# Kernel tuning notes

Measured on AMD Instinct MI355X. Metric: run time of the kernel, lower is better.

Reference implementation:

```python
import jax, jax.numpy as jnp
import numpy as np

B, Fc, C, H, D, L = 128, 256, 256, 8, 32, 6  # batch, columns, dim, heads, head_dim, layers


def _ln(x, g, b, eps=1e-5):
    m = x.mean(-1, keepdims=True)
    v = ((x - m) ** 2).mean(-1, keepdims=True)
    return (x - m) * jax.lax.rsqrt(v + eps) * g + b


def setup_inputs() -> dict:
    key = jax.random.key(0)
    ks = jax.random.split(key, 16)
    s = 0.02  # weight init scale to keep 6-layer activations stable
    return {
        "x": jax.random.normal(ks[0], (B, Fc, C), jnp.float32),
        "col_emb": jax.random.normal(ks[1], (1, Fc, C), jnp.float32),
        "pos_emb": jax.random.normal(ks[2], (1, Fc + 1, C), jnp.float32),
        "col_bias": jax.random.normal(ks[3], (Fc, Fc), jnp.float32),
        "ln1_g": jnp.ones((L, C), jnp.float32),
        "ln1_b": jnp.zeros((L, C), jnp.float32),
        "qkv_w": jax.random.normal(ks[4], (L, C, 3 * C), jnp.float32) * s,
        "qkv_b": jnp.zeros((L, 3 * C), jnp.float32),
        "out_w": jax.random.normal(ks[5], (L, C, C), jnp.float32) * s,
        "out_b": jnp.zeros((L, C), jnp.float32),
        "ln2_g": jnp.ones((L, C), jnp.float32),
        "ln2_b": jnp.zeros((L, C), jnp.float32),
        "w1": jax.random.normal(ks[6], (L, C, 4 * C), jnp.float32) * s,
        "b1": jnp.zeros((L, 4 * C), jnp.float32),
        "w2": jax.random.normal(ks[7], (L, 4 * C, 2 * C), jnp.float32) * s,
        "b2": jnp.zeros((L, 2 * C), jnp.float32),
        "w3": jax.random.normal(ks[8], (L, C, C), jnp.float32) * s,
        "b3": jnp.zeros((L, C), jnp.float32),
        "fin_g": jnp.ones((C,), jnp.float32),
        "fin_b": jnp.zeros((C,), jnp.float32),
    }


def reference(x, col_emb, pos_emb, col_bias, ln1_g, ln1_b, qkv_w, qkv_b,
              out_w, out_b, ln2_g, ln2_b, w1, b1, w2, b2, w3, b3, fin_g, fin_b):
    Fdim = x.shape[1]
    h = x + col_emb[:, :Fdim] + pos_emb[:, 1:Fdim + 1]
    bias = col_bias[:Fdim, :Fdim]  # [T, T]
    scale = 1.0 / np.sqrt(D).astype(np.float32)
    params = (ln1_g, ln1_b, qkv_w, qkv_b, out_w, out_b, ln2_g, ln2_b,
              w1, b1, w2, b2, w3, b3)

    def block(xc, p):
        g1, be1, qw, qb, ow, ob, g2, be2, W1, B1, W2, B2, W3, B3 = p
        Bn, T, Cd = xc.shape
        hn = _ln(xc, g1, be1)
        qkv = hn @ qw + qb                              # [B,T,3C]
        q, k, v = jnp.split(qkv, 3, axis=-1)
        q = q.reshape(Bn, T, H, D)
        k = k.reshape(Bn, T, H, D)
        v = v.reshape(Bn, T, H, D)
        scores = jnp.einsum('bthd,bshd->bhts', q, k) * scale + bias[None, None]
        w = jax.nn.softmax(scores, axis=-1)             # dropout = identity (eval)
        attn = jnp.einsum('bhts,bshd->bthd', w, v).reshape(Bn, T, Cd)
        attn = attn @ ow + ob
        attn = attn + bias[None]                        # [1,T,T] broadcast, T==C
        xc = xc + attn
        hn2 = _ln(xc, g2, be2)
        u = jax.nn.gelu(hn2 @ W1 + B1, approximate=False)
        gl = u @ W2 + B2                                # [B,T,2C]
        a, gate = jnp.split(gl, 2, axis=-1)
        xc = xc + (a * jax.nn.sigmoid(gate)) @ W3 + B3
        return xc, None

    h, _ = jax.lax.scan(block, h, params)
    h = _ln(h, fin_g, fin_b)
    return h.mean(axis=1)  # pooling='mean' -> [B, C]
```

## Files before the change

kernel.cpp:

```cpp
#include <hip/hip_runtime.h>

typedef __bf16 bx8 __attribute__((ext_vector_type(8)));
typedef float fx4 __attribute__((ext_vector_type(4)));

#define GAS(p) ((const __attribute__((address_space(1))) void*)(const void*)(p))
#define LAS(p) ((__attribute__((address_space(3))) void*)(void*)(p))
#define WAITVM(n) do { asm volatile("s_waitcnt vmcnt(" #n ")" ::: "memory"); \
                       __builtin_amdgcn_sched_barrier(0); } while (0)
#define WAITLG0() do { asm volatile("s_waitcnt lgkmcnt(0)" ::: "memory"); \
                       __builtin_amdgcn_sched_barrier(0); } while (0)

__device__ __forceinline__ unsigned short f2bf(float f) {
  return __builtin_bit_cast(unsigned short, (__bf16)f);
}

__global__ __launch_bounds__(256) void wtrans_kernel(const float* __restrict__ src,
                                                     unsigned short* __restrict__ dst,
                                                     int K, int N) {
  __shared__ unsigned short t[64][68];
  const int l = blockIdx.z;
  const float* s = src + (size_t)l * K * N;
  unsigned short* d = dst + (size_t)l * N * K;
  const int n0 = blockIdx.x * 64, k0 = blockIdx.y * 64;
  const int tx = threadIdx.x & 63, ty = threadIdx.x >> 6;
#pragma unroll
  for (int r = 0; r < 64; r += 4)
    t[tx][ty + r] = f2bf(s[(size_t)(k0 + ty + r) * N + n0 + tx]);
  __syncthreads();
#pragma unroll
  for (int r = 0; r < 64; r += 4)
    d[(size_t)(n0 + ty + r) * K + k0 + tx] = t[ty + r][tx];
}

__global__ __launch_bounds__(256) void embed_ln_kernel(const float4* __restrict__ x,
                                                       const float4* __restrict__ ce,
                                                       const float4* __restrict__ pe,
                                                       const float* __restrict__ gw,
                                                       const float* __restrict__ bw,
                                                       float4* __restrict__ xres,
                                                       unsigned short* __restrict__ hn) {
  const int row = blockIdx.x * 4 + (threadIdx.x >> 6);
  const int lane = threadIdx.x & 63;
  const int t = row & 255;
  const size_t idx = (size_t)row * 64 + lane;
  float4 a = x[idx], b = ce[t * 64 + lane], p = pe[(t + 1) * 64 + lane];
  float4 v = make_float4(a.x + b.x + p.x, a.y + b.y + p.y, a.z + b.z + p.z, a.w + b.w + p.w);
  xres[idx] = v;
  float s = v.x + v.y + v.z + v.w;
  float q = v.x * v.x + v.y * v.y + v.z * v.z + v.w * v.w;
#pragma unroll
  for (int off = 1; off < 64; off <<= 1) {
    s += __shfl_xor(s, off);
    q += __shfl_xor(q, off);
  }
  float mean = s * (1.0f / 256.0f);
  float rs = rsqrtf(q * (1.0f / 256.0f) - mean * mean + 1e-5f);
  float4 gv = *(const float4*)(gw + lane * 4);
  float4 bv = *(const float4*)(bw + lane * 4);
  ushort4 o;
  o.x = f2bf((v.x - mean) * rs * gv.x + bv.x);
  o.y = f2bf((v.y - mean) * rs * gv.y + bv.y);
  o.z = f2bf((v.z - mean) * rs * gv.z + bv.z);
  o.w = f2bf((v.w - mean) * rs * gv.w + bv.w);
  *(ushort4*)(hn + (size_t)row * 256 + lane * 4) = o;
}

__global__ __launch_bounds__(256) void mean_part_kernel(const float* __restrict__ x,
                                                        const float2* __restrict__ stats,
                                                        float* __restrict__ part) {
  int b = blockIdx.x, half = blockIdx.y, c = threadIdx.x;
  const float* xb = x + (size_t)b * 65536 + half * 32768;
  const float2* st = stats + b * 256 + half * 128;
  float acc = 0.f;
#pragma unroll 4
  for (int t = 0; t < 128; ++t) {
    float2 s = st[t];
    acc += (xb[t * 256 + c] - s.x) * s.y;
  }
  part[(size_t)(b * 2 + half) * 256 + c] = acc;
}
__global__ __launch_bounds__(256) void mean_fin_kernel(const float* __restrict__ part,
                                                       const float* __restrict__ fg,
                                                       const float* __restrict__ fb,
                                                       float* __restrict__ out) {
  int b = blockIdx.x, c = threadIdx.x;
  out[b * 256 + c] =
      (part[(size_t)(2 * b) * 256 + c] + part[(size_t)(2 * b + 1) * 256 + c]) *
          (1.0f / 256.0f) * fg[c] + fb[c];
}

template <int EP>
__global__ __launch_bounds__(256) void gemm_kernel(const unsigned short* __restrict__ A,
                                                   const unsigned short* __restrict__ BT,
                                                   const float* __restrict__ bvec,
                                                   float* __restrict__ resid,
                                                   unsigned short* __restrict__ outb,
                                                   int N, int K) {
  __shared__ unsigned short lA[2][128 * 32];
  __shared__ unsigned short lB[2][128 * 32];
  const int tid = threadIdx.x;
  const int lane = tid & 63, w = tid >> 6;
  const int wr = w >> 1, wc = w & 1;
  const int g = lane >> 4, lr = lane & 15;
  const int m0 = blockIdx.y * 128, n0 = blockIdx.x * 128;
  fx4 acc[4][4] = {};

  auto STAGE = [&](int buf, int kk) {
#pragma unroll
    for (int r = 0; r < 2; ++r) {
      int u = r * 256 + tid;
      int row = u >> 2, sl = u & 3;
      int c = sl ^ ((row >> 1) & 3);
      __builtin_amdgcn_global_load_lds(GAS(A + (size_t)(m0 + row) * K + kk + c * 8),
                                       LAS(&lA[buf][u * 8]), 16, 0, 0);
      __builtin_amdgcn_global_load_lds(GAS(BT + (size_t)(n0 + row) * K + kk + c * 8),
                                       LAS(&lB[buf][u * 8]), 16, 0, 0);
    }
  };

  const int nt = K >> 5;
  STAGE(0, 0);
  STAGE(1, 32);
  for (int t = 0; t < nt; ++t) {
    if (t == nt - 1) WAITVM(0); else WAITVM(4);
    __builtin_amdgcn_s_barrier();
    const int buf = t & 1;
    bx8 af[4], bq[4];
#pragma unroll
    for (int i = 0; i < 4; ++i) {
      int row = wr * 64 + i * 16 + lr;
      af[i] = *(const bx8*)&lA[buf][row * 32 + (g ^ ((row >> 1) & 3)) * 8];
      int col = wc * 64 + i * 16 + lr;
      bq[i] = *(const bx8*)&lB[buf][col * 32 + (g ^ ((col >> 1) & 3)) * 8];
    }
    WAITLG0();
    __builtin_amdgcn_s_barrier();
    if (t + 2 < nt) STAGE(buf, (t + 2) * 32);
#pragma unroll
    for (int i = 0; i < 4; ++i)
#pragma unroll
      for (int j = 0; j < 4; ++j)
        acc[i][j] = __builtin_amdgcn_mfma_f32_16x16x32_bf16(bq[j], af[i], acc[i][j], 0, 0, 0);
  }

#pragma unroll
  for (int i = 0; i < 4; ++i) {
    const int m = m0 + wr * 64 + i * 16 + lr;
#pragma unroll
    for (int j = 0; j < 4; ++j) {
      const int nc = n0 + wc * 64 + j * 16 + g * 4;
      const float4 bv = *(const float4*)(bvec + nc);
      float v0 = acc[i][j][0] + bv.x, v1 = acc[i][j][1] + bv.y;
      float v2 = acc[i][j][2] + bv.z, v3 = acc[i][j][3] + bv.w;
      if constexpr (EP == 1) {
        v0 = 0.5f * v0 * (1.0f + erff(v0 * 0.70710678118654752f));
        v1 = 0.5f * v1 * (1.0f + erff(v1 * 0.70710678118654752f));
        v2 = 0.5f * v2 * (1.0f + erff(v2 * 0.70710678118654752f));
        v3 = 0.5f * v3 * (1.0f + erff(v3 * 0.70710678118654752f));
      }
      if constexpr (EP == 1) {
        ushort4 st;
        st.x = f2bf(v0); st.y = f2bf(v1); st.z = f2bf(v2); st.w = f2bf(v3);
        *(ushort4*)(outb + (size_t)m * N + nc) = st;
      } else {
        if (nc < 512) {
          ushort4 st;
          st.x = f2bf(v0); st.y = f2bf(v1); st.z = f2bf(v2); st.w = f2bf(v3);
          *(ushort4*)(outb + (size_t)m * N + nc) = st;
        } else {
          unsigned short* vTp = (unsigned short*)resid;
          const int s = m & 255, b = m >> 8;
          const int hv = nc - 512;
          const int h = hv >> 5, d0 = hv & 31;
          const int jj = (s & 3) + 4 * ((s >> 4) & 1);
          const int ub = (s >> 5) * 128 + ((s >> 2) & 3) * 32 + d0;
          unsigned short* base = vTp + (size_t)(b * 8 + h) * 8192;
          const float vv[4] = {v0, v1, v2, v3};
#pragma unroll
          for (int r = 0; r < 4; ++r) {
            int u = ub + r;
            int up = (u & ~7) | ((u & 7) ^ ((u >> 3) & 7));
            base[up * 8 + jj] = f2bf(vv[r]);
          }
        }
      }
    }
  }
}

template <int EP, int LNM>
__global__ __launch_bounds__(256) void gemm_ln_kernel(const unsigned short* __restrict__ A,
                                                      const unsigned short* __restrict__ BT,
                                                      const float* __restrict__ bvec,
                                                      const float* __restrict__ cbias,
                                                      float* __restrict__ resid,
                                                      const float* __restrict__ lnw,
                                                      const float* __restrict__ lnb,
                                                      unsigned short* __restrict__ hn,
                                                      float2* __restrict__ stats,
                                                      int K) {
  __shared__ unsigned short lA[2][32 * 32];
  __shared__ unsigned short lB[2][256 * 32];
  __shared__ float2 red[4][32];
  const int tid = threadIdx.x;
  const int lane = tid & 63, w = tid >> 6;
  const int g = lane >> 4, lr = lane & 15;
  const int m0 = blockIdx.x * 32;
  fx4 acc[2][4] = {};

  auto STAGE = [&](int buf, int kk) {
    {
      int u = tid & 127;
      int row = u >> 2, sl = u & 3;
      int c = sl ^ ((row >> 1) & 3);
      __builtin_amdgcn_global_load_lds(GAS(A + (size_t)(m0 + row) * K + kk + c * 8),
                                       LAS(&lA[buf][u * 8]), 16, 0, 0);
    }
#pragma unroll
    for (int r = 0; r < 4; ++r) {
      int u = r * 256 + tid;
      int row = u >> 2, sl = u & 3;
      int c = sl ^ ((row >> 1) & 3);
      __builtin_amdgcn_global_load_lds(GAS(BT + (size_t)row * K + kk + c * 8),
                                       LAS(&lB[buf][u * 8]), 16, 0, 0);
    }
  };

  const int nt = K >> 5;
  STAGE(0, 0);
  STAGE(1, 32);
  for (int t = 0; t < nt; ++t) {
    if (t == nt - 1) WAITVM(0); else WAITVM(5);
    __builtin_amdgcn_s_barrier();
    const int buf = t & 1;
    bx8 af[2], bq[4];
#pragma unroll
    for (int i = 0; i < 2; ++i) {
      int row = i * 16 + lr;
      af[i] = *(const bx8*)&lA[buf][row * 32 + (g ^ ((row >> 1) & 3)) * 8];
    }
#pragma unroll
    for (int j = 0; j < 4; ++j) {
      int col = w * 64 + j * 16 + lr;
      bq[j] = *(const bx8*)&lB[buf][col * 32 + (g ^ ((col >> 1) & 3)) * 8];
    }
    WAITLG0();
    __builtin_amdgcn_s_barrier();
    if (t + 2 < nt) STAGE(buf, (t + 2) * 32);
#pragma unroll
    for (int i = 0; i < 2; ++i)
#pragma unroll
      for (int j = 0; j < 4; ++j)
        acc[i][j] = __builtin_amdgcn_mfma_f32_16x16x32_bf16(bq[j], af[i], acc[i][j], 0, 0, 0);
  }

  float s[2] = {0.f, 0.f}, q[2] = {0.f, 0.f};
#pragma unroll
  for (int i = 0; i < 2; ++i) {
    const int m = m0 + i * 16 + lr;
#pragma unroll
    for (int j = 0; j < 4; ++j) {
      const int nc = w * 64 + j * 16 + g * 4;
      const float4 bv = *(const float4*)(bvec + nc);
      float v0 = acc[i][j][0] + bv.x, v1 = acc[i][j][1] + bv.y;
      float v2 = acc[i][j][2] + bv.z, v3 = acc[i][j][3] + bv.w;
      if constexpr (EP == 2) {
        const float4 cb = *(const float4*)(cbias + (size_t)(m & 255) * 256 + nc);
        v0 += cb.x; v1 += cb.y; v2 += cb.z; v3 += cb.w;
      }
      float4* rp = (float4*)(resid + (size_t)m * 256 + nc);
      float4 old = *rp;
      v0 += old.x; v1 += old.y; v2 += old.z; v3 += old.w;
      *rp = make_float4(v0, v1, v2, v3);
      acc[i][j][0] = v0; acc[i][j][1] = v1; acc[i][j][2] = v2; acc[i][j][3] = v3;
      s[i] += v0 + v1 + v2 + v3;
      q[i] += v0 * v0 + v1 * v1 + v2 * v2 + v3 * v3;
    }
  }
#pragma unroll
  for (int i = 0; i < 2; ++i) {
    s[i] += __shfl_xor(s[i], 16); s[i] += __shfl_xor(s[i], 32);
    q[i] += __shfl_xor(q[i], 16); q[i] += __shfl_xor(q[i], 32);
  }
  if (lane < 16) {
#pragma unroll
    for (int i = 0; i < 2; ++i) red[w][i * 16 + lr] = make_float2(s[i], q[i]);
  }
  __syncthreads();
  float mean[2], rs[2];
#pragma unroll
  for (int i = 0; i < 2; ++i) {
    float2 r0 = red[0][i * 16 + lr], r1 = red[1][i * 16 + lr];
    float2 r2 = red[2][i * 16 + lr], r3 = red[3][i * 16 + lr];
    float S = r0.x + r1.x + r2.x + r3.x;
    float Q = r0.y + r1.y + r2.y + r3.y;
    mean[i] = S * (1.0f / 256.0f);
    rs[i] = rsqrtf(Q * (1.0f / 256.0f) - mean[i] * mean[i] + 1e-5f);
  }
  if constexpr (LNM == 1) {
    if (w == 0 && g == 0) {
#pragma unroll
      for (int i = 0; i < 2; ++i) stats[m0 + i * 16 + lr] = make_float2(mean[i], rs[i]);
    }
  } else {
#pragma unroll
    for (int i = 0; i < 2; ++i) {
      const int m = m0 + i * 16 + lr;
#pragma unroll
      for (int j = 0; j < 4; ++j) {
        const int nc = w * 64 + j * 16 + g * 4;
        const float4 gv = *(const float4*)(lnw + nc);
        const float4 bv2 = *(const float4*)(lnb + nc);
        ushort4 st;
        st.x = f2bf((acc[i][j][0] - mean[i]) * rs[i] * gv.x + bv2.x);
        st.y = f2bf((acc[i][j][1] - mean[i]) * rs[i] * gv.y + bv2.y);
        st.z = f2bf((acc[i][j][2] - mean[i]) * rs[i] * gv.z + bv2.z);
        st.w = f2bf((acc[i][j][3] - mean[i]) * rs[i] * gv.w + bv2.w);
        *(ushort4*)(hn + (size_t)m * 256 + nc) = st;
      }
    }
  }
}

__global__ __launch_bounds__(256) void gemm_w2f64_kernel(const unsigned short* __restrict__ A,
                                                         const unsigned short* __restrict__ BT,
                                                         const float* __restrict__ b2,
                                                         unsigned short* __restrict__ gout) {
  __shared__ unsigned short lA[3][64 * 32];
  __shared__ unsigned short lBa[3][128 * 32];
  __shared__ unsigned short lBg[3][128 * 32];
  const int tid = threadIdx.x;
  const int lane = tid & 63, w = tid >> 6;
  const int g = lane >> 4, lr = lane & 15;
  const int m0 = blockIdx.y * 64, n0 = blockIdx.x * 128;
  fx4 aA[4][2] = {}, aG[4][2] = {};

  auto STAGE = [&](int buf, int kk) {
    {
      int u = tid;
      int row = u >> 2, sl = u & 3;
      int c = sl ^ ((row >> 1) & 3);
      __builtin_amdgcn_global_load_lds(GAS(A + (size_t)(m0 + row) * 1024 + kk + c * 8),
                                       LAS(&lA[buf][u * 8]), 16, 0, 0);
    }
#pragma unroll
    for (int r = 0; r < 2; ++r) {
      int u = r * 256 + tid;
      int row = u >> 2, sl = u & 3;
      int c = sl ^ ((row >> 1) & 3);
      __builtin_amdgcn_global_load_lds(GAS(BT + (size_t)(n0 + row) * 1024 + kk + c * 8),
                                       LAS(&lBa[buf][u * 8]), 16, 0, 0);
      __builtin_amdgcn_global_load_lds(GAS(BT + (size_t)(256 + n0 + row) * 1024 + kk + c * 8),
                                       LAS(&lBg[buf][u * 8]), 16, 0, 0);
    }
  };

  STAGE(0, 0);
  STAGE(1, 32);
  STAGE(2, 64);
  int buf = 0;
  for (int t = 0; t < 32; ++t) {
    if (t < 30) WAITVM(10); else if (t == 30) WAITVM(5); else WAITVM(0);
    __builtin_amdgcn_s_barrier();
    bx8 af[4], ba[2], bg[2];
#pragma unroll
    for (int i = 0; i < 4; ++i) {
      int row = i * 16 + lr;
      af[i] = *(const bx8*)&lA[buf][row * 32 + (g ^ ((row >> 1) & 3)) * 8];
    }
#pragma unroll
    for (int j = 0; j < 2; ++j) {
      int col = w * 32 + j * 16 + lr;
      int sw = (g ^ ((col >> 1) & 3)) * 8;
      ba[j] = *(const bx8*)&lBa[buf][col * 32 + sw];
      bg[j] = *(const bx8*)&lBg[buf][col * 32 + sw];
    }
    WAITLG0();
    __builtin_amdgcn_s_barrier();
    if (t + 3 < 32) STAGE(buf, (t + 3) * 32);
#pragma unroll
    for (int i = 0; i < 4; ++i)
#pragma unroll
      for (int j = 0; j < 2; ++j) {
        aA[i][j] = __builtin_amdgcn_mfma_f32_16x16x32_bf16(ba[j], af[i], aA[i][j], 0, 0, 0);
        aG[i][j] = __builtin_amdgcn_mfma_f32_16x16x32_bf16(bg[j], af[i], aG[i][j], 0, 0, 0);
      }
    buf = (buf == 2) ? 0 : buf + 1;
  }

#pragma unroll
  for (int i = 0; i < 4; ++i) {
    const int m = m0 + i * 16 + lr;
#pragma unroll
    for (int j = 0; j < 2; ++j) {
      const int nc = n0 + w * 32 + j * 16 + g * 4;
      const float4 bva = *(const float4*)(b2 + nc);
      const float4 bvg = *(const float4*)(b2 + 256 + nc);
      float a0 = aA[i][j][0] + bva.x, a1 = aA[i][j][1] + bva.y;
      float a2 = aA[i][j][2] + bva.z, a3 = aA[i][j][3] + bva.w;
      float g0 = aG[i][j][0] + bvg.x, g1 = aG[i][j][1] + bvg.y;
      float g2 = aG[i][j][2] + bvg.z, g3 = aG[i][j][3] + bvg.w;
      ushort4 st;
      st.x = f2bf(a0 / (1.0f + __expf(-g0)));
      st.y = f2bf(a1 / (1.0f + __expf(-g1)));
      st.z = f2bf(a2 / (1.0f + __expf(-g2)));
      st.w = f2bf(a3 / (1.0f + __expf(-g3)));
      *(ushort4*)(gout + (size_t)m * 256 + nc) = st;
    }
  }
}

__global__ __launch_bounds__(256) void attn_kernel(const unsigned short* __restrict__ qkv,
                                                   const unsigned short* __restrict__ vT,
                                                   const float* __restrict__ cbias,
                                                   unsigned short* __restrict__ attnb) {
  __shared__ unsigned short Kl[256 * 32];
  __shared__ unsigned short Vl[1024 * 8];
  const int bh = blockIdx.x, b = bh >> 3, h = bh & 7;
  const int tid = threadIdx.x, lane = tid & 63, w = tid >> 6;
  const int g = lane >> 4, lr = lane & 15;
  const unsigned short* qb_ = qkv + (size_t)b * 196608;
  const unsigned short* vTb = vT + (size_t)bh * 8192;
#pragma unroll
  for (int r = 0; r < 4; ++r) {
    int u = r * 256 + tid;
    int s = u >> 2, sl = u & 3;
    int c = sl ^ ((s >> 1) & 3);
    __builtin_amdgcn_global_load_lds(GAS(qb_ + (size_t)s * 768 + 256 + h * 32 + c * 8),
                                     LAS(&Kl[u * 8]), 16, 0, 0);
    __builtin_amdgcn_global_load_lds(GAS(vTb + u * 8), LAS(&Vl[u * 8]), 16, 0, 0);
  }
  asm volatile("s_waitcnt vmcnt(0)" ::: "memory");
  __syncthreads();
  const float scale = 0.17677669529663689f;
  const fx4 zero = {0.f, 0.f, 0.f, 0.f};
#pragma unroll 1
  for (int it = 0; it < 4; ++it) {
    const int t = it * 64 + w * 16 + lr;
    bx8 qf = *(const bx8*)(qb_ + (size_t)t * 768 + h * 32 + g * 8);
    float p[16][4];
    float mx = -1e30f;
#pragma unroll
    for (int n = 0; n < 16; ++n) {
      int sr = n * 16 + lr;
      bx8 kf = *(const bx8*)&Kl[sr * 32 + (g ^ ((sr >> 1) & 3)) * 8];
      fx4 sc = __builtin_amdgcn_mfma_f32_16x16x32_bf16(kf, qf, zero, 0, 0, 0);
      const float4 cb = *(const float4*)(cbias + (size_t)t * 256 + n * 16 + g * 4);
      p[n][0] = sc[0] * scale + cb.x;
      p[n][1] = sc[1] * scale + cb.y;
      p[n][2] = sc[2] * scale + cb.z;
      p[n][3] = sc[3] * scale + cb.w;
      mx = fmaxf(mx, fmaxf(fmaxf(p[n][0], p[n][1]), fmaxf(p[n][2], p[n][3])));
    }
    mx = fmaxf(mx, __shfl_xor(mx, 16));
    mx = fmaxf(mx, __shfl_xor(mx, 32));
    float sum = 0.f;
    bx8 bq[8];
#pragma unroll
    for (int c = 0; c < 8; ++c) {
      union { bx8 v; unsigned short u[8]; } pk;
#pragma unroll
      for (int jj = 0; jj < 8; ++jj) {
        float e = __expf(p[2 * c + (jj >> 2)][jj & 3] - mx);
        sum += e;
        pk.u[jj] = f2bf(e);
      }
      bq[c] = pk.v;
    }
    sum += __shfl_xor(sum, 16);
    sum += __shfl_xor(sum, 32);
    const float inv = 1.0f / sum;
    fx4 oa0 = zero, oa1 = zero;
#pragma unroll
    for (int c = 0; c < 8; ++c) {
      int u0 = c * 128 + g * 32 + lr;
      int u0p = (u0 & ~7) | ((u0 & 7) ^ ((u0 >> 3) & 7));
      bx8 vf0 = *(const bx8*)&Vl[u0p * 8];
      oa0 = __builtin_amdgcn_mfma_f32_16x16x32_bf16(vf0, bq[c], oa0, 0, 0, 0);
      int u1 = u0 + 16;
      int u1p = (u1 & ~7) | ((u1 & 7) ^ ((u1 >> 3) & 7));
      bx8 vf1 = *(const bx8*)&Vl[u1p * 8];
      oa1 = __builtin_amdgcn_mfma_f32_16x16x32_bf16(vf1, bq[c], oa1, 0, 0, 0);
    }
    ushort4 o0, o1;
    o0.x = f2bf(oa0[0] * inv); o0.y = f2bf(oa0[1] * inv);
    o0.z = f2bf(oa0[2] * inv); o0.w = f2bf(oa0[3] * inv);
    o1.x = f2bf(oa1[0] * inv); o1.y = f2bf(oa1[1] * inv);
    o1.z = f2bf(oa1[2] * inv); o1.w = f2bf(oa1[3] * inv);
    unsigned short* orow = attnb + (size_t)(b * 256 + t) * 256 + h * 32;
    *(ushort4*)(orow + 4 * g) = o0;
    *(ushort4*)(orow + 16 + 4 * g) = o1;
  }
}

extern "C" void kernel_launch(void* const* d_in, const int* in_sizes, int n_in,
                              void* d_out, int out_size, void* d_ws, size_t ws_size,
                              hipStream_t stream) {
  (void)in_sizes; (void)n_in; (void)out_size; (void)ws_size;
  const float* x     = (const float*)d_in[0];
  const float* cemb  = (const float*)d_in[1];
  const float* pemb  = (const float*)d_in[2];
  const float* cbias = (const float*)d_in[3];
  const float* ln1g  = (const float*)d_in[4];
  const float* ln1b  = (const float*)d_in[5];
  const float* qkvw  = (const float*)d_in[6];
  const float* qkvb  = (const float*)d_in[7];
  const float* outw  = (const float*)d_in[8];
  const float* outbv = (const float*)d_in[9];
  const float* ln2g  = (const float*)d_in[10];
  const float* ln2b  = (const float*)d_in[11];
  const float* w1    = (const float*)d_in[12];
  const float* b1    = (const float*)d_in[13];
  const float* w2    = (const float*)d_in[14];
  const float* b2    = (const float*)d_in[15];
  const float* w3    = (const float*)d_in[16];
  const float* b3    = (const float*)d_in[17];
  const float* fing  = (const float*)d_in[18];
  const float* finb  = (const float*)d_in[19];

  char* ws = (char*)d_ws;
  float* x_res = (float*)(ws);
  unsigned short* hn   = (unsigned short*)(ws + 33554432);
  unsigned short* big  = (unsigned short*)(ws + 50331648);
  unsigned short* vT   = (unsigned short*)(ws + 100663296);
  unsigned short* wT   = (unsigned short*)(ws + 117440512);
  float2* stats = (float2*)(ws + 130809856);
  float* part  = (float*)big;

  unsigned short* qkvwT = wT;
  unsigned short* outwT = wT + 1179648;
  unsigned short* w1T   = wT + 1572864;
  unsigned short* w2T   = wT + 3145728;
  unsigned short* w3T   = wT + 6291456;

  wtrans_kernel<<<dim3(12, 4, 6), 256, 0, stream>>>(qkvw, qkvwT, 256, 768);
  wtrans_kernel<<<dim3(4, 4, 6), 256, 0, stream>>>(outw, outwT, 256, 256);
  wtrans_kernel<<<dim3(16, 4, 6), 256, 0, stream>>>(w1, w1T, 256, 1024);
  wtrans_kernel<<<dim3(8, 16, 6), 256, 0, stream>>>(w2, w2T, 1024, 512);
  wtrans_kernel<<<dim3(4, 4, 6), 256, 0, stream>>>(w3, w3T, 256, 256);
  embed_ln_kernel<<<8192, 256, 0, stream>>>((const float4*)x, (const float4*)cemb,
                                            (const float4*)pemb, ln1g, ln1b,
                                            (float4*)x_res, hn);
  for (int l = 0; l < 6; ++l) {
    gemm_kernel<4><<<dim3(6, 256), 256, 0, stream>>>(hn, qkvwT + (size_t)l * 196608,
                                                     qkvb + l * 768, (float*)vT, big,
                                                     768, 256);
    attn_kernel<<<1024, 256, 0, stream>>>(big, vT, cbias, hn);
    gemm_ln_kernel<2, 0><<<1024, 256, 0, stream>>>(hn, outwT + (size_t)l * 65536,
                                                   outbv + l * 256, cbias, x_res,
                                                   ln2g + l * 256, ln2b + l * 256, hn,
                                                   nullptr, 256);
    gemm_kernel<1><<<dim3(8, 256), 256, 0, stream>>>(hn, w1T + (size_t)l * 262144,
                                                     b1 + l * 1024, nullptr, big,
                                                     1024, 256);
    gemm_w2f64_kernel<<<dim3(2, 512), 256, 0, stream>>>(big, w2T + (size_t)l * 524288,
                                                        b2 + l * 512, hn);
    if (l < 5) {
      gemm_ln_kernel<3, 0><<<1024, 256, 0, stream>>>(hn, w3T + (size_t)l * 65536,
                                                     b3 + l * 256, nullptr, x_res,
                                                     ln1g + (l + 1) * 256,
                                                     ln1b + (l + 1) * 256, hn,
                                                     nullptr, 256);
    } else {
      gemm_ln_kernel<3, 1><<<1024, 256, 0, stream>>>(hn, w3T + (size_t)l * 65536,
                                                     b3 + l * 256, nullptr, x_res,
                                                     nullptr, nullptr, nullptr,
                                                     stats, 256);
    }
  }
  mean_part_kernel<<<dim3(128, 2), 256, 0, stream>>>(x_res, stats, part);
  mean_fin_kernel<<<128, 256, 0, stream>>>(part, fing, finb, (float*)d_out);
}
```

Baseline: 1.487 ms.

## Use 64-row GEMM tiles and triple-buffer LDS staging in GEMM kernels

The QKV and W1 GEMMs now use 64x128 tiles instead of 128x128, which doubles the grid size. Each warp now covers 64 rows by 32 columns. Both the generic GEMM and the GEMM+LayerNorm kernels move from double to triple-buffered LDS prefetch, with adjusted vmcnt waits and a rotating buffer index. The aim is more blocks per GPU and deeper latency hiding for the short K=256 loops, at the cost of more LDS per block and lower per-block reuse of B tiles.

```diff
diff --git a/kernel.cpp b/kernel.cpp
--- a/kernel.cpp
+++ b/kernel.cpp
@@ -90,29 +90,33 @@
 }
 
 template <int EP>
-__global__ __launch_bounds__(256) void gemm_kernel(const unsigned short* __restrict__ A,
-                                                   const unsigned short* __restrict__ BT,
-                                                   const float* __restrict__ bvec,
-                                                   float* __restrict__ resid,
-                                                   unsigned short* __restrict__ outb,
-                                                   int N, int K) {
-  __shared__ unsigned short lA[2][128 * 32];
-  __shared__ unsigned short lB[2][128 * 32];
+__global__ __launch_bounds__(256) void gemm64_kernel(const unsigned short* __restrict__ A,
+                                                     const unsigned short* __restrict__ BT,
+                                                     const float* __restrict__ bvec,
+                                                     float* __restrict__ resid,
+                                                     unsigned short* __restrict__ outb,
+                                                     int N, int K) {
+  __shared__ unsigned short lA[3][64 * 32];
+  __shared__ unsigned short lB[3][128 * 32];
   const int tid = threadIdx.x;
   const int lane = tid & 63, w = tid >> 6;
-  const int wr = w >> 1, wc = w & 1;
   const int g = lane >> 4, lr = lane & 15;
-  const int m0 = blockIdx.y * 128, n0 = blockIdx.x * 128;
-  fx4 acc[4][4] = {};
+  const int m0 = blockIdx.y * 64, n0 = blockIdx.x * 128;
+  fx4 acc[4][2] = {};
 
   auto STAGE = [&](int buf, int kk) {
+    {
+      int u = tid;
+      int row = u >> 2, sl = u & 3;
+      int c = sl ^ ((row >> 1) & 3);
+      __builtin_amdgcn_global_load_lds(GAS(A + (size_t)(m0 + row) * K + kk + c * 8),
+                                       LAS(&lA[buf][u * 8]), 16, 0, 0);
+    }
 #pragma unroll
     for (int r = 0; r < 2; ++r) {
       int u = r * 256 + tid;
       int row = u >> 2, sl = u & 3;
       int c = sl ^ ((row >> 1) & 3);
-      __builtin_amdgcn_global_load_lds(GAS(A + (size_t)(m0 + row) * K + kk + c * 8),
-                                       LAS(&lA[buf][u * 8]), 16, 0, 0);
       __builtin_amdgcn_global_load_lds(GAS(BT + (size_t)(n0 + row) * K + kk + c * 8),
                                        LAS(&lB[buf][u * 8]), 16, 0, 0);
     }
@@ -121,34 +125,39 @@
   const int nt = K >> 5;
   STAGE(0, 0);
   STAGE(1, 32);
+  STAGE(2, 64);
+  int buf = 0;
   for (int t = 0; t < nt; ++t) {
-    if (t == nt - 1) WAITVM(0); else WAITVM(4);
+    if (t < nt - 2) WAITVM(6); else if (t == nt - 2) WAITVM(3); else WAITVM(0);
     __builtin_amdgcn_s_barrier();
-    const int buf = t & 1;
-    bx8 af[4], bq[4];
+    bx8 af[4], bq[2];
 #pragma unroll
     for (int i = 0; i < 4; ++i) {
-      int row = wr * 64 + i * 16 + lr;
+      int row = i * 16 + lr;
       af[i] = *(const bx8*)&lA[buf][row * 32 + (g ^ ((row >> 1) & 3)) * 8];
-      int col = wc * 64 + i * 16 + lr;
-      bq[i] = *(const bx8*)&lB[buf][col * 32 + (g ^ ((col >> 1) & 3)) * 8];
+    }
+#pragma unroll
+    for (int j = 0; j < 2; ++j) {
+      int col = w * 32 + j * 16 + lr;
+      bq[j] = *(const bx8*)&lB[buf][col * 32 + (g ^ ((col >> 1) & 3)) * 8];
     }
     WAITLG0();
     __builtin_amdgcn_s_barrier();
-    if (t + 2 < nt) STAGE(buf, (t + 2) * 32);
+    if (t + 3 < nt) STAGE(buf, (t + 3) * 32);
 #pragma unroll
     for (int i = 0; i < 4; ++i)
 #pragma unroll
-      for (int j = 0; j < 4; ++j)
+      for (int j = 0; j < 2; ++j)
         acc[i][j] = __builtin_amdgcn_mfma_f32_16x16x32_bf16(bq[j], af[i], acc[i][j], 0, 0, 0);
+    buf = (buf == 2) ? 0 : buf + 1;
   }
 
 #pragma unroll
   for (int i = 0; i < 4; ++i) {
-    const int m = m0 + wr * 64 + i * 16 + lr;
-#pragma unroll
-    for (int j = 0; j < 4; ++j) {
-      const int nc = n0 + wc * 64 + j * 16 + g * 4;
+    const int m = m0 + i * 16 + lr;
+#pragma unroll
+    for (int j = 0; j < 2; ++j) {
+      const int nc = n0 + w * 32 + j * 16 + g * 4;
       const float4 bv = *(const float4*)(bvec + nc);
       float v0 = acc[i][j][0] + bv.x, v1 = acc[i][j][1] + bv.y;
       float v2 = acc[i][j][2] + bv.z, v3 = acc[i][j][3] + bv.w;
@@ -199,8 +208,8 @@
                                                       unsigned short* __restrict__ hn,
                                                       float2* __restrict__ stats,
                                                       int K) {
-  __shared__ unsigned short lA[2][32 * 32];
-  __shared__ unsigned short lB[2][256 * 32];
+  __shared__ unsigned short lA[3][32 * 32];
+  __shared__ unsigned short lB[3][256 * 32];
   __shared__ float2 red[4][32];
   const int tid = threadIdx.x;
   const int lane = tid & 63, w = tid >> 6;
@@ -229,10 +238,11 @@
   const int nt = K >> 5;
   STAGE(0, 0);
   STAGE(1, 32);
+  STAGE(2, 64);
+  int buf = 0;
   for (int t = 0; t < nt; ++t) {
-    if (t == nt - 1) WAITVM(0); else WAITVM(5);
+    if (t < nt - 2) WAITVM(10); else if (t == nt - 2) WAITVM(5); else WAITVM(0);
     __builtin_amdgcn_s_barrier();
-    const int buf = t & 1;
     bx8 af[2], bq[4];
 #pragma unroll
     for (int i = 0; i < 2; ++i) {
@@ -246,12 +256,13 @@
     }
     WAITLG0();
     __builtin_amdgcn_s_barrier();
-    if (t + 2 < nt) STAGE(buf, (t + 2) * 32);
+    if (t + 3 < nt) STAGE(buf, (t + 3) * 32);
 #pragma unroll
     for (int i = 0; i < 2; ++i)
 #pragma unroll
       for (int j = 0; j < 4; ++j)
         acc[i][j] = __builtin_amdgcn_mfma_f32_16x16x32_bf16(bq[j], af[i], acc[i][j], 0, 0, 0);
+    buf = (buf == 2) ? 0 : buf + 1;
   }
 
   float s[2] = {0.f, 0.f}, q[2] = {0.f, 0.f};
@@ -542,17 +553,17 @@
                                             (const float4*)pemb, ln1g, ln1b,
                                             (float4*)x_res, hn);
   for (int l = 0; l < 6; ++l) {
-    gemm_kernel<4><<<dim3(6, 256), 256, 0, stream>>>(hn, qkvwT + (size_t)l * 196608,
-                                                     qkvb + l * 768, (float*)vT, big,
-                                                     768, 256);
+    gemm64_kernel<4><<<dim3(6, 512), 256, 0, stream>>>(hn, qkvwT + (size_t)l * 196608,
+                                                       qkvb + l * 768, (float*)vT, big,
+                                                       768, 256);
     attn_kernel<<<1024, 256, 0, stream>>>(big, vT, cbias, hn);
     gemm_ln_kernel<2, 0><<<1024, 256, 0, stream>>>(hn, outwT + (size_t)l * 65536,
                                                    outbv + l * 256, cbias, x_res,
                                                    ln2g + l * 256, ln2b + l * 256, hn,
                                                    nullptr, 256);
-    gemm_kernel<1><<<dim3(8, 256), 256, 0, stream>>>(hn, w1T + (size_t)l * 262144,
-                                                     b1 + l * 1024, nullptr, big,
-                                                     1024, 256);
+    gemm64_kernel<1><<<dim3(8, 512), 256, 0, stream>>>(hn, w1T + (size_t)l * 262144,
+                                                       b1 + l * 1024, nullptr, big,
+                                                       1024, 256);
     gemm_w2f64_kernel<<<dim3(2, 512), 256, 0, stream>>>(big, w2T + (size_t)l * 524288,
                                                         b2 + l * 512, hn);
     if (l < 5) {
```

After: 1.508 ms. No clear change (+1.4%).
